# Optimization experiments

Measured on AMD Instinct MI355X. Metric: run time of the kernel, lower is better.

## Reference

```python
import jax, jax.numpy as jnp
import numpy as np

B, T, S, D, V = 32, 2048, 256, 1024, 56
STAR_PENALTY = -1.0
NEG = -1e30  # -inf surrogate that is safe for gradients


def setup_inputs() -> dict:
    key = jax.random.key(0)
    k1, k2, k3 = jax.random.split(key, 3)
    features = jax.random.normal(k1, (B, T, D), jnp.float32)
    targets = jax.random.randint(k2, (B, S), 1, V)  # 0 is the blank; labels in [1, V)
    W = jax.random.normal(k3, (V, D), jnp.float32) * (1.0 / 32.0)  # 1/sqrt(D)
    b = jnp.zeros((V,), jnp.float32)
    input_lengths = jnp.full((B,), T, jnp.int32)
    target_lengths = jnp.full((B,), S, jnp.int32)
    return dict(features=features, W=W, b=b, targets=targets,
                input_lengths=input_lengths, target_lengths=target_lengths)


def _star_ctc_losses(logp, targets, input_lengths, target_lengths, star_penalty):
    """Star-CTC forward (DP) score.
    logp: (T, N, C) log-softmax emissions; targets: (N, S) labels (blank=0 excluded).
    Extended state sequence [*, t1, *, t2, ..., tS, *]: star states play the role of
    CTC blanks but act as penalized wildcards, emitting logsumexp(logp)+star_penalty
    (== star_penalty for normalized log-probs). Standard CTC transition topology:
    self-loop, advance by 1, advance by 2 into a token state when it differs from the
    previous token. Returns per-sequence negative log-likelihood, shape (N,)."""
    Tlen, N, C = logp.shape
    Slen = targets.shape[1]
    L = 2 * Slen + 1
    ext = jnp.zeros((N, L), targets.dtype).at[:, 1::2].set(targets)  # (N, L)
    is_star = (jnp.arange(L) % 2 == 0)[None, :]                      # (1, L)
    prev2 = jnp.pad(ext[:, :-2], ((0, 0), (2, 0)), constant_values=-1)
    allow_skip = (~is_star) & (ext != prev2)                         # (N, L)

    def emit(logp_t):  # logp_t: (N, C) -> (N, L)
        star_e = star_penalty + jax.nn.logsumexp(logp_t, axis=-1, keepdims=True)
        tok_e = jnp.take_along_axis(logp_t, ext, axis=-1)
        return jnp.where(is_star, star_e, tok_e)

    alpha0 = jnp.where(jnp.arange(L)[None, :] < 2, emit(logp[0]), NEG)

    def step(alpha, xs):
        logp_t, t = xs
        a1 = jnp.pad(alpha[:, :-1], ((0, 0), (1, 0)), constant_values=NEG)
        a2 = jnp.where(allow_skip,
                       jnp.pad(alpha[:, :-2], ((0, 0), (2, 0)), constant_values=NEG),
                       NEG)
        new = jnp.logaddexp(jnp.logaddexp(alpha, a1), a2) + emit(logp_t)
        new = jnp.where(t < input_lengths[:, None], new, alpha)  # freeze past input_length
        return new, None

    alpha, _ = jax.lax.scan(step, alpha0, (logp[1:], jnp.arange(1, Tlen)))
    last = 2 * target_lengths                  # index of the final star state
    rows = jnp.arange(N)
    score = jnp.logaddexp(alpha[rows, last], alpha[rows, last - 1])
    return -score


def reference(features, W, b, targets, input_lengths, target_lengths):
    # classifier + log_softmax (Dropout(0.2) is identity at eval time)
    logits = jnp.einsum('btd,vd->btv', features, W) + b
    logp = jax.nn.log_softmax(logits.astype(jnp.float32), axis=-1)
    logp = jnp.transpose(logp, (1, 0, 2))      # (T, N, C) as in logits.permute(1,0,2)
    losses = _star_ctc_losses(logp, targets, input_lengths, target_lengths, STAR_PENALTY)
    # ctc_reduce_mean: length-normalized mean loss
    return jnp.mean(losses / target_lengths.astype(losses.dtype))
```

## Files before the change

### kernel.cpp

```cpp
#include <hip/hip_runtime.h>
#include <hip/hip_bf16.h>
#include <math.h>

typedef __attribute__((ext_vector_type(4))) float f32x4;
typedef __attribute__((ext_vector_type(8))) short s16x8;

#define LOG2E 1.4426950408889634f
#define LN2f  0.6931471805599453f
#define INV_E 0.36787944117144233f

__device__ __forceinline__ short bfc(float x) {
  unsigned u = __float_as_uint(x);
  unsigned r = u + 0x7fffu + ((u >> 16) & 1u);
  return (short)(r >> 16);
}

__device__ __forceinline__ unsigned pk2(float x, float y) {
  union { __hip_bfloat162 h; unsigned u; } c;
  c.h = __float22bfloat162_rn(make_float2(x, y));
  return c.u;
}

__device__ __forceinline__ float rdlane(float v, int lane) {
  return __int_as_float(__builtin_amdgcn_readlane(__float_as_int(v), lane));
}

__device__ __forceinline__ float pick9(int j, float a0, float a1, float a2,
                                       float a3, float a4, float a5, float a6,
                                       float a7, float a8) {
  float v = a0;
  if (j == 1) v = a1;
  if (j == 2) v = a2;
  if (j == 3) v = a3;
  if (j == 4) v = a4;
  if (j == 5) v = a5;
  if (j == 6) v = a6;
  if (j == 7) v = a7;
  if (j == 8) v = a8;
  return v;
}

__global__ void conv_w(const float* __restrict__ W, short* __restrict__ Wb,
                       int V, int D) {
  int idx = blockIdx.x * blockDim.x + threadIdx.x;
  if (idx >= 64 * D) return;
  int row = idx / D, col = idx - row * D;
  Wb[idx] = (row < V) ? bfc(W[(size_t)row * D + col]) : (short)0;
}

__global__ __launch_bounds__(256, 1) void fused_gemm_star(
    const float* __restrict__ feat, const short* __restrict__ Wb,
    const float* __restrict__ bias, float* __restrict__ ptg,
    float* __restrict__ skb, int* __restrict__ flags,
    const int* __restrict__ targets, const int* __restrict__ in_len,
    const int* __restrict__ tgt_len, float* __restrict__ partial,
    int nrows, int D, int V, int T, int S, int B, int CPB) {

  __shared__ float gbuf[4][4][64];

  if ((int)blockIdx.x >= B) {
    const int NPROD = gridDim.x - B;
    const int NTILES = B * CPB;
    const int lane = threadIdx.x & 63;
    const int wave = threadIdx.x >> 6;
    const int m_lo = lane & 15;
    const int q = lane >> 4;
    const size_t bstr = (size_t)16 * D;

    for (int i = blockIdx.x - B; i < NTILES; i += NPROD) {
      const int c = i / B;
      const int b = i - c * B;
      const int tc0 = c * 128;
      const int rlen = (T - tc0 < 128) ? (T - tc0) : 128;
      const int rowlim = b * T + tc0 + rlen;
      const int rowbase = b * T + tc0 + wave * 32;

      const int* tg = targets + (size_t)b * S;
      const int l0 = lane * 4;
      const int g1 = (l0 < S) ? tg[l0] : 0;
      const int g3 = (l0 + 1 < S) ? tg[l0 + 1] : 0;
      const int g5 = (l0 + 2 < S) ? tg[l0 + 2] : 0;
      const int g7 = (l0 + 3 < S) ? tg[l0 + 3] : 0;

      int arow0 = rowbase + m_lo;
      int arow1 = rowbase + 16 + m_lo;
      if (arow0 >= nrows) arow0 = nrows - 1;
      if (arow1 >= nrows) arow1 = nrows - 1;
      const short* Bp = Wb + (size_t)m_lo * D + q * 8;

      f32x4 acc[2][4];
      #pragma unroll
      for (int g = 0; g < 2; ++g)
        #pragma unroll
        for (int ni = 0; ni < 4; ++ni) acc[g][ni] = (f32x4){0.f, 0.f, 0.f, 0.f};

      const float* Ap0 = feat + (size_t)arow0 * D + q * 8;
      const float* Ap1 = feat + (size_t)arow1 * D + q * 8;
      float4 al0 = *(const float4*)(Ap0);
      float4 ah0 = *(const float4*)(Ap0 + 4);
      float4 al1 = *(const float4*)(Ap1);
      float4 ah1 = *(const float4*)(Ap1 + 4);
      s16x8 b0 = *(const s16x8*)(Bp);
      s16x8 b1 = *(const s16x8*)(Bp + bstr);
      s16x8 b2 = *(const s16x8*)(Bp + 2 * bstr);
      s16x8 b3 = *(const s16x8*)(Bp + 3 * bstr);

      for (int k0 = 0; k0 < D; k0 += 32) {
        const int kn = (k0 + 32 < D) ? (k0 + 32) : 0;
        const float* Ap0n = feat + (size_t)arow0 * D + kn + q * 8;
        const float* Ap1n = feat + (size_t)arow1 * D + kn + q * 8;
        const short* Bpn = Wb + (size_t)m_lo * D + kn + q * 8;
        float4 nal0 = *(const float4*)(Ap0n);
        float4 nah0 = *(const float4*)(Ap0n + 4);
        float4 nal1 = *(const float4*)(Ap1n);
        float4 nah1 = *(const float4*)(Ap1n + 4);
        s16x8 nb0 = *(const s16x8*)(Bpn);
        s16x8 nb1 = *(const s16x8*)(Bpn + bstr);
        s16x8 nb2 = *(const s16x8*)(Bpn + 2 * bstr);
        s16x8 nb3 = *(const s16x8*)(Bpn + 3 * bstr);

        union { s16x8 v; unsigned u[4]; } av0, av1;
        av0.u[0] = pk2(al0.x, al0.y); av0.u[1] = pk2(al0.z, al0.w);
        av0.u[2] = pk2(ah0.x, ah0.y); av0.u[3] = pk2(ah0.z, ah0.w);
        av1.u[0] = pk2(al1.x, al1.y); av1.u[1] = pk2(al1.z, al1.w);
        av1.u[2] = pk2(ah1.x, ah1.y); av1.u[3] = pk2(ah1.z, ah1.w);

        acc[0][0] = __builtin_amdgcn_mfma_f32_16x16x32_bf16(av0.v, b0, acc[0][0], 0, 0, 0);
        acc[0][1] = __builtin_amdgcn_mfma_f32_16x16x32_bf16(av0.v, b1, acc[0][1], 0, 0, 0);
        acc[0][2] = __builtin_amdgcn_mfma_f32_16x16x32_bf16(av0.v, b2, acc[0][2], 0, 0, 0);
        acc[0][3] = __builtin_amdgcn_mfma_f32_16x16x32_bf16(av0.v, b3, acc[0][3], 0, 0, 0);
        acc[1][0] = __builtin_amdgcn_mfma_f32_16x16x32_bf16(av1.v, b0, acc[1][0], 0, 0, 0);
        acc[1][1] = __builtin_amdgcn_mfma_f32_16x16x32_bf16(av1.v, b1, acc[1][1], 0, 0, 0);
        acc[1][2] = __builtin_amdgcn_mfma_f32_16x16x32_bf16(av1.v, b2, acc[1][2], 0, 0, 0);
        acc[1][3] = __builtin_amdgcn_mfma_f32_16x16x32_bf16(av1.v, b3, acc[1][3], 0, 0, 0);

        al0 = nal0; ah0 = nah0; al1 = nal1; ah1 = nah1;
        b0 = nb0; b1 = nb1; b2 = nb2; b3 = nb3;
      }

      float bias_v[4];
      #pragma unroll
      for (int ni = 0; ni < 4; ++ni) {
        int col = ni * 16 + m_lo;
        bias_v[ni] = (col < V) ? bias[col] : 0.f;
      }

      #pragma unroll
      for (int g = 0; g < 2; ++g) {
        #pragma unroll
        for (int r = 0; r < 4; ++r) {
          float lg[4];
          #pragma unroll
          for (int ni = 0; ni < 4; ++ni) {
            int col = ni * 16 + m_lo;
            lg[ni] = (col < V) ? (acc[g][ni][r] + bias_v[ni]) : -1e30f;
          }
          float m = fmaxf(fmaxf(lg[0], lg[1]), fmaxf(lg[2], lg[3]));
          #pragma unroll
          for (int off = 1; off < 16; off <<= 1) m = fmaxf(m, __shfl_xor(m, off));
          float p[4];
          #pragma unroll
          for (int ni = 0; ni < 4; ++ni) p[ni] = exp2f((lg[ni] - m) * LOG2E);
          float s = (p[0] + p[1]) + (p[2] + p[3]);
          #pragma unroll
          for (int off = 1; off < 16; off <<= 1) s += __shfl_xor(s, off);

          #pragma unroll
          for (int ni = 0; ni < 4; ++ni)
            gbuf[wave][q][ni * 16 + m_lo] = p[ni];

          #pragma unroll
          for (int rr = 0; rr < 4; ++rr) {
            int grow = rowbase + g * 16 + rr * 4 + r;
            if (grow < rowlim) {
              float srow = rdlane(s, rr * 16);
              float4 ev;
              ev.x = gbuf[wave][rr][g1];
              ev.y = gbuf[wave][rr][g3];
              ev.z = gbuf[wave][rr][g5];
              ev.w = gbuf[wave][rr][g7];
              *(float4*)(ptg + ((size_t)grow * 64 + lane) * 4) = ev;
              if (lane == 0) {
                float2 skv;
                skv.x = srow * INV_E;
                skv.y = logf(srow);
                *(float2*)(skb + (size_t)grow * 2) = skv;
              }
            }
          }
        }
      }

      __syncthreads();
      if (threadIdx.x == 0)
        __hip_atomic_store(&flags[b * CPB + c], 1, __ATOMIC_RELEASE,
                           __HIP_MEMORY_SCOPE_AGENT);
    }
    return;
  }

  if (threadIdx.x >= 64) return;
  const int n = blockIdx.x;
  const int lane = threadIdx.x;
  const int len = in_len[n];
  const int tl = tgt_len[n];
  const int* tg = targets + (size_t)n * S;
  const int* fl = flags + n * CPB;
  const float* prow = ptg + (size_t)n * T * 256;
  const float* srow = skb + (size_t)n * T * 2;

  int cdone = -1;
#define WAITC(cc)                                                            \
  do {                                                                       \
    int _c = (cc);                                                           \
    if (cdone < _c) {                                                        \
      while (cdone < _c) {                                                   \
        if (__hip_atomic_load((int*)&fl[cdone + 1], __ATOMIC_RELAXED,        \
                              __HIP_MEMORY_SCOPE_AGENT))                     \
          ++cdone;                                                           \
        else                                                                 \
          __builtin_amdgcn_s_sleep(8);                                       \
      }                                                                      \
      __builtin_amdgcn_fence(__ATOMIC_ACQUIRE, "agent");                     \
    }                                                                        \
  } while (0)

  const int s0 = lane * 4;
  int lab1 = (s0     < S) ? tg[s0]     : 0;
  int lab3 = (s0 + 1 < S) ? tg[s0 + 1] : 0;
  int lab5 = (s0 + 2 < S) ? tg[s0 + 2] : 0;
  int lab7 = (s0 + 3 < S) ? tg[s0 + 3] : 0;
  int labm1 = __shfl_up(lab7, 1);
  int labm3 = __shfl_up(lab5, 1);
  const bool sk1 = (lane > 0) && (lab1 != labm1);
  const bool sk3 = (lab3 != lab1);
  const bool sk5 = (lab5 != lab3);
  const bool sk7 = (lab7 != lab5);
  const bool skm1 = (labm1 != labm3);

  float a0 = 0, a1 = 0, a2 = 0, a3 = 0, a4 = 0, a5 = 0, a6 = 0, a7 = 0, a8 = 0;
  float m1 = 0.f, m2 = 0.f, m3 = 0.f;
  int eps = 0, eL = 0;
  bool act = (lane == 0);

#define PTGL(t) (*(const float4*)(prow +                                     \
    ((size_t)(((t) < len) ? (t) : (len - 1)) * 256 + lane * 4)))
#define SKLL(t) (*(const float2*)(srow +                                     \
    ((size_t)(((t) < len) ? (t) : (len - 1)) * 2)))

  WAITC(0);

  float4 r0 = PTGL(0);
  float2 k0v = SKLL(0);
  if (lane == 0) { a0 = k0v.x; a1 = r0.x; }
  float ksum = k0v.y;

  float4 rr0 = PTGL(1), rr1 = PTGL(2), rr2 = PTGL(3), rr3 = PTGL(4);
  float4 rr4 = PTGL(5), rr5 = PTGL(6), rr6 = PTGL(7), rr7 = PTGL(8);
  float2 kr0 = SKLL(1), kr1 = SKLL(2), kr2 = SKLL(3), kr3 = SKLL(4);
  float2 kr4 = SKLL(5), kr5 = SKLL(6), kr6 = SKLL(7), kr7 = SKLL(8);

  float em1a = __shfl_up(rr0.w, 1);

#define RENORM()                                                             \
  do {                                                                       \
    float mx = fmaxf(fmaxf(fmaxf(a0, a1), fmaxf(a2, a3)),                    \
                     fmaxf(fmaxf(a4, a5), fmaxf(a6, a7)));                   \
    mx = fmaxf(mx, a8);                                                      \
    int e = (int)((__float_as_uint(mx) >> 23) & 255) - 126;                  \
    e = (act && mx > 0.f) ? e : 0;                                           \
    a0 = ldexpf(a0, -e); a1 = ldexpf(a1, -e); a2 = ldexpf(a2, -e);           \
    a3 = ldexpf(a3, -e); a4 = ldexpf(a4, -e); a5 = ldexpf(a5, -e);           \
    a6 = ldexpf(a6, -e); a7 = ldexpf(a7, -e); a8 = ldexpf(a8, -e);           \
    eps += e;                                                                \
  } while (0)

#define PAIR(EC0, EC1, KC0, KC1, NX, P0, P1, DOREN)                          \
  do {                                                                       \
    ksum += KC0.y; ksum += KC1.y;                                            \
    if (!act) eps = eL;                                                      \
    bool inc = (lane != 0) &&                                                \
               ((m1 != 0.f) || (m2 != 0.f) || (m3 != 0.f));                  \
    int d = inc ? (eL - eps) : 0;                                            \
    if (__builtin_expect(d > 24, 0)) {                  \
      a0 = ldexpf(a0, -d); a1 = ldexpf(a1, -d); a2 = ldexpf(a2, -d);         \
      a3 = ldexpf(a3, -d); a4 = ldexpf(a4, -d); a5 = ldexpf(a5, -d);         \
      a6 = ldexpf(a6, -d); a7 = ldexpf(a7, -d); a8 = ldexpf(a8, -d);         \
      eps += d;                                      \
    } else {                                                                 \
      m1 = ldexpf(m1, d); m2 = ldexpf(m2, d); m3 = ldexpf(m3, d);            \
    }                                                                        \
    act = act || (m1 != 0.f) || (m2 != 0.f) || (m3 != 0.f);                  \
                  \
    a8 = (a8 + a7) * KC0.x;                                                  \
    a7 = (a7 + a6 + (sk7 ? a5 : 0.f)) * EC0.w;                               \
    a6 = (a6 + a5) * KC0.x;                                                  \
    a5 = (a5 + a4 + (sk5 ? a3 : 0.f)) * EC0.z;                               \
    a4 = (a4 + a3) * KC0.x;                                                  \
    a3 = (a3 + a2 + (sk3 ? a1 : 0.f)) * EC0.y;                               \
    a2 = (a2 + a1) * KC0.x;                                                  \
    a1 = (a1 + a0 + (sk1 ? m1 : 0.f)) * EC0.x;                               \
    a0 = (a0 + m1) * KC0.x;                                                  \
    m1 = (m1 + m2 + (skm1 ? m3 : 0.f)) * em1a;                               \
                                                             \
    a8 = (a8 + a7) * KC1.x;                                                  \
    a7 = (a7 + a6 + (sk7 ? a5 : 0.f)) * EC1.w;                               \
    a6 = (a6 + a5) * KC1.x;                                                  \
    a5 = (a5 + a4 + (sk5 ? a3 : 0.f)) * EC1.z;                               \
    a4 = (a4 + a3) * KC1.x;                                                  \
    a3 = (a3 + a2 + (sk3 ? a1 : 0.f)) * EC1.y;                               \
    a2 = (a2 + a1) * KC1.x;                                                  \
    a1 = (a1 + a0 + (sk1 ? m1 : 0.f)) * EC1.x;                               \
    a0 = (a0 + m1) * KC1.x;                                                  \
    EC0 = PTGL(P0); EC1 = PTGL(P1);                   \
    KC0 = SKLL(P0); KC1 = SKLL(P1);                                          \
    if (DOREN) RENORM();                                                     \
    em1a = __shfl_up(NX.w, 1);                     \
                          \
    m3 = __shfl_up(a5, 1); m2 = __shfl_up(a6, 1); m1 = __shfl_up(a7, 1);     \
    eL = __shfl_up(eps, 1);                                                  \
    if (lane == 0) { m1 = 0.f; m2 = 0.f; m3 = 0.f; }                         \
  } while (0)

  int t0 = 1;
  for (; t0 + 8 <= len; t0 += 8) {
    int tmax = t0 + 15;
    if (tmax > len - 1) tmax = len - 1;
    WAITC(tmax >> 7);
    PAIR(rr0, rr1, kr0, kr1, rr2, t0 + 8,  t0 + 9,  false);
    PAIR(rr2, rr3, kr2, kr3, rr4, t0 + 10, t0 + 11, false);
    PAIR(rr4, rr5, kr4, kr5, rr6, t0 + 12, t0 + 13, false);
    PAIR(rr6, rr7, kr6, kr7, rr0, t0 + 14, t0 + 15, true);
  }

  WAITC((len - 1) >> 7);

  for (int t = t0; t < len; ++t) {
    float4 cv = PTGL(t);
    float2 kc = SKLL(t);
    ksum += kc.y;
    if (!act) eps = eL;
    bool inc = (lane != 0) && (m1 != 0.f);
    int d = inc ? (eL - eps) : 0;
    float m1s;
    if (__builtin_expect(d > 24, 0)) {
      a0 = ldexpf(a0, -d); a1 = ldexpf(a1, -d); a2 = ldexpf(a2, -d);
      a3 = ldexpf(a3, -d); a4 = ldexpf(a4, -d); a5 = ldexpf(a5, -d);
      a6 = ldexpf(a6, -d); a7 = ldexpf(a7, -d); a8 = ldexpf(a8, -d);
      eps += d; m1s = m1;
    } else {
      m1s = inc ? ldexpf(m1, d) : 0.f;
    }
    act = act || (m1s != 0.f);
    a8 = (a8 + a7) * kc.x;
    a7 = (a7 + a6 + (sk7 ? a5 : 0.f)) * cv.w;
    a6 = (a6 + a5) * kc.x;
    a5 = (a5 + a4 + (sk5 ? a3 : 0.f)) * cv.z;
    a4 = (a4 + a3) * kc.x;
    a3 = (a3 + a2 + (sk3 ? a1 : 0.f)) * cv.y;
    a2 = (a2 + a1) * kc.x;
    a1 = (a1 + a0 + (sk1 ? m1s : 0.f)) * cv.x;
    a0 = (a0 + m1s) * kc.x;
    if ((t & 7) == 0) RENORM();
    m1 = __shfl_up(a7, 1);
    eL = __shfl_up(eps, 1);
    if (lane == 0) m1 = 0.f;
  }

  int last = 2 * tl;
  int kx = last >> 3, jx = last & 7;
  if (kx > 63) { kx = 63; jx = last - 504; }
  int ky = (last - 1) >> 3, jy = (last - 1) & 7;
  float vx = pick9(jx, a0, a1, a2, a3, a4, a5, a6, a7, a8);
  float vy = pick9(jy, a0, a1, a2, a3, a4, a5, a6, a7, a8);
  float sx = __shfl(vx, kx); int ex = __shfl(eps, kx);
  float sy = __shfl(vy, ky); int ey = __shfl(eps, ky);
  if (lane == 0) {
    int em = (ex > ey) ? ex : ey;
    float v = ldexpf(sx, ex - em) + ldexpf(sy, ey - em);
    float score = logf(v) + (float)em * LN2f - ksum;
    partial[n] = -score / (float)tl;
  }
#undef WAITC
#undef PTGL
#undef SKLL
#undef RENORM
#undef PAIR
}

__global__ void reduce_mean(const float* __restrict__ partial,
                            float* __restrict__ out, int B) {
  float v = 0.f;
  for (int i = threadIdx.x; i < B; i += 64) v += partial[i];
  #pragma unroll
  for (int off = 32; off > 0; off >>= 1) v += __shfl_down(v, off, 64);
  if (threadIdx.x == 0) out[0] = v / (float)B;
}

extern "C" void kernel_launch(void* const* d_in, const int* in_sizes, int n_in,
                              void* d_out, int out_size, void* d_ws, size_t ws_size,
                              hipStream_t stream) {
  const float* feat = (const float*)d_in[0];
  const float* W = (const float*)d_in[1];
  const float* bias = (const float*)d_in[2];
  const int* targets = (const int*)d_in[3];
  const int* in_len = (const int*)d_in[4];
  const int* tgt_len = (const int*)d_in[5];
  float* out = (float*)d_out;

  const int V = in_sizes[2];
  const int D = in_sizes[1] / V;
  const int B = in_sizes[4];
  const int T = in_sizes[0] / (B * D);
  const int S = in_sizes[3] / B;
  const int nrows = B * T;

  float* ptg = (float*)d_ws;
  float* skb = ptg + (size_t)nrows * 256;
  float* partial = skb + (size_t)nrows * 2;
  short* Wb = (short*)(partial + B);
  const int CPB = (T + 127) / 128;
  int* flags = (int*)((char*)Wb + (size_t)64 * D * sizeof(short));

  hipMemsetAsync(flags, 0, (size_t)B * CPB * sizeof(int), stream);

  conv_w<<<(64 * D + 255) / 256, 256, 0, stream>>>(W, Wb, V, D);

  int NPROD = 256 - B;
  const int NTILES = B * CPB;
  if (NPROD > NTILES) NPROD = NTILES;
  fused_gemm_star<<<dim3(B + NPROD), 256, 0, stream>>>(
      feat, Wb, bias, ptg, skb, flags, targets, in_len, tgt_len, partial,
      nrows, D, V, T, S, B, CPB);

  reduce_mean<<<1, 64, 0, stream>>>(partial, out, B);
}
```

Measured before the change: 715.1 us.

## Launch one producer block per tile with deeper load prefetch and fused flag reset

Producer blocks no longer loop over tiles persistently: the grid now has one block per (batch, chunk) tile, and launch bounds allow two blocks per CU. The GEMM K-loop keeps a four-stage register prefetch instead of one stage, so more global loads are in flight to hide memory latency. The flag memset is folded into the weight-conversion kernel to drop a separate launch. The risk is scheduling: consumer blocks spin-wait on flags, so if producer blocks are dispatched ahead of consumers or starve them, forward progress depends on dispatch order. Register pressure also rises from the extra prefetch buffers while the occupancy target is higher.

```diff
diff --git a/kernel.cpp b/kernel.cpp
--- a/kernel.cpp
+++ b/kernel.cpp
@@ -41,14 +41,15 @@
 }
 
 __global__ void conv_w(const float* __restrict__ W, short* __restrict__ Wb,
-                       int V, int D) {
+                       int V, int D, int* __restrict__ flags, int nflags) {
   int idx = blockIdx.x * blockDim.x + threadIdx.x;
+  if (idx < nflags) flags[idx] = 0;
   if (idx >= 64 * D) return;
   int row = idx / D, col = idx - row * D;
   Wb[idx] = (row < V) ? bfc(W[(size_t)row * D + col]) : (short)0;
 }
 
-__global__ __launch_bounds__(256, 1) void fused_gemm_star(
+__global__ __launch_bounds__(256, 2) void fused_gemm_star(
     const float* __restrict__ feat, const short* __restrict__ Wb,
     const float* __restrict__ bias, float* __restrict__ ptg,
     float* __restrict__ skb, int* __restrict__ flags,
@@ -59,143 +60,149 @@
   __shared__ float gbuf[4][4][64];
 
   if ((int)blockIdx.x >= B) {
-    const int NPROD = gridDim.x - B;
-    const int NTILES = B * CPB;
+    const int j = blockIdx.x - B;
+    const int c = j / B;
+    const int b = j - c * B;
+    const int tc0 = c * 128;
+    const int rlen = (T - tc0 < 128) ? (T - tc0) : 128;
+    const int rowlim = b * T + tc0 + rlen;
+
     const int lane = threadIdx.x & 63;
     const int wave = threadIdx.x >> 6;
     const int m_lo = lane & 15;
     const int q = lane >> 4;
     const size_t bstr = (size_t)16 * D;
-
-    for (int i = blockIdx.x - B; i < NTILES; i += NPROD) {
-      const int c = i / B;
-      const int b = i - c * B;
-      const int tc0 = c * 128;
-      const int rlen = (T - tc0 < 128) ? (T - tc0) : 128;
-      const int rowlim = b * T + tc0 + rlen;
-      const int rowbase = b * T + tc0 + wave * 32;
-
-      const int* tg = targets + (size_t)b * S;
-      const int l0 = lane * 4;
-      const int g1 = (l0 < S) ? tg[l0] : 0;
-      const int g3 = (l0 + 1 < S) ? tg[l0 + 1] : 0;
-      const int g5 = (l0 + 2 < S) ? tg[l0 + 2] : 0;
-      const int g7 = (l0 + 3 < S) ? tg[l0 + 3] : 0;
-
-      int arow0 = rowbase + m_lo;
-      int arow1 = rowbase + 16 + m_lo;
-      if (arow0 >= nrows) arow0 = nrows - 1;
-      if (arow1 >= nrows) arow1 = nrows - 1;
-      const short* Bp = Wb + (size_t)m_lo * D + q * 8;
-
-      f32x4 acc[2][4];
+    const int rowbase = b * T + tc0 + wave * 32;
+
+    const int* tg = targets + (size_t)b * S;
+    const int l0 = lane * 4;
+    const int g1 = (l0 < S) ? tg[l0] : 0;
+    const int g3 = (l0 + 1 < S) ? tg[l0 + 1] : 0;
+    const int g5 = (l0 + 2 < S) ? tg[l0 + 2] : 0;
+    const int g7 = (l0 + 3 < S) ? tg[l0 + 3] : 0;
+
+    int arow0 = rowbase + m_lo;
+    int arow1 = rowbase + 16 + m_lo;
+    if (arow0 >= nrows) arow0 = nrows - 1;
+    if (arow1 >= nrows) arow1 = nrows - 1;
+    const float* A0base = feat + (size_t)arow0 * D + q * 8;
+    const float* A1base = feat + (size_t)arow1 * D + q * 8;
+    const short* Bbase = Wb + (size_t)m_lo * D + q * 8;
+
+    f32x4 acc[2][4];
+    #pragma unroll
+    for (int g = 0; g < 2; ++g)
       #pragma unroll
-      for (int g = 0; g < 2; ++g)
-        #pragma unroll
-        for (int ni = 0; ni < 4; ++ni) acc[g][ni] = (f32x4){0.f, 0.f, 0.f, 0.f};
-
-      const float* Ap0 = feat + (size_t)arow0 * D + q * 8;
-      const float* Ap1 = feat + (size_t)arow1 * D + q * 8;
-      float4 al0 = *(const float4*)(Ap0);
-      float4 ah0 = *(const float4*)(Ap0 + 4);
-      float4 al1 = *(const float4*)(Ap1);
-      float4 ah1 = *(const float4*)(Ap1 + 4);
-      s16x8 b0 = *(const s16x8*)(Bp);
-      s16x8 b1 = *(const s16x8*)(Bp + bstr);
-      s16x8 b2 = *(const s16x8*)(Bp + 2 * bstr);
-      s16x8 b3 = *(const s16x8*)(Bp + 3 * bstr);
-
-      for (int k0 = 0; k0 < D; k0 += 32) {
-        const int kn = (k0 + 32 < D) ? (k0 + 32) : 0;
-        const float* Ap0n = feat + (size_t)arow0 * D + kn + q * 8;
-        const float* Ap1n = feat + (size_t)arow1 * D + kn + q * 8;
-        const short* Bpn = Wb + (size_t)m_lo * D + kn + q * 8;
-        float4 nal0 = *(const float4*)(Ap0n);
-        float4 nah0 = *(const float4*)(Ap0n + 4);
-        float4 nal1 = *(const float4*)(Ap1n);
-        float4 nah1 = *(const float4*)(Ap1n + 4);
-        s16x8 nb0 = *(const s16x8*)(Bpn);
-        s16x8 nb1 = *(const s16x8*)(Bpn + bstr);
-        s16x8 nb2 = *(const s16x8*)(Bpn + 2 * bstr);
-        s16x8 nb3 = *(const s16x8*)(Bpn + 3 * bstr);
-
-        union { s16x8 v; unsigned u[4]; } av0, av1;
-        av0.u[0] = pk2(al0.x, al0.y); av0.u[1] = pk2(al0.z, al0.w);
-        av0.u[2] = pk2(ah0.x, ah0.y); av0.u[3] = pk2(ah0.z, ah0.w);
-        av1.u[0] = pk2(al1.x, al1.y); av1.u[1] = pk2(al1.z, al1.w);
-        av1.u[2] = pk2(ah1.x, ah1.y); av1.u[3] = pk2(ah1.z, ah1.w);
-
-        acc[0][0] = __builtin_amdgcn_mfma_f32_16x16x32_bf16(av0.v, b0, acc[0][0], 0, 0, 0);
-        acc[0][1] = __builtin_amdgcn_mfma_f32_16x16x32_bf16(av0.v, b1, acc[0][1], 0, 0, 0);
-        acc[0][2] = __builtin_amdgcn_mfma_f32_16x16x32_bf16(av0.v, b2, acc[0][2], 0, 0, 0);
-        acc[0][3] = __builtin_amdgcn_mfma_f32_16x16x32_bf16(av0.v, b3, acc[0][3], 0, 0, 0);
-        acc[1][0] = __builtin_amdgcn_mfma_f32_16x16x32_bf16(av1.v, b0, acc[1][0], 0, 0, 0);
-        acc[1][1] = __builtin_amdgcn_mfma_f32_16x16x32_bf16(av1.v, b1, acc[1][1], 0, 0, 0);
-        acc[1][2] = __builtin_amdgcn_mfma_f32_16x16x32_bf16(av1.v, b2, acc[1][2], 0, 0, 0);
-        acc[1][3] = __builtin_amdgcn_mfma_f32_16x16x32_bf16(av1.v, b3, acc[1][3], 0, 0, 0);
-
-        al0 = nal0; ah0 = nah0; al1 = nal1; ah1 = nah1;
-        b0 = nb0; b1 = nb1; b2 = nb2; b3 = nb3;
-      }
-
-      float bias_v[4];
+      for (int ni = 0; ni < 4; ++ni) acc[g][ni] = (f32x4){0.f, 0.f, 0.f, 0.f};
+
+#define DECLS(s) float4 al0_##s, ah0_##s, al1_##s, ah1_##s;                  \
+                 s16x8 b0_##s, b1_##s, b2_##s, b3_##s
+    DECLS(0); DECLS(1); DECLS(2); DECLS(3);
+#undef DECLS
+
+#define LOADS(s, kk)                                                         \
+  do {                                                                       \
+    const float* A0p = A0base + (kk);                                        \
+    const float* A1p = A1base + (kk);                                        \
+    const short* Bpp = Bbase + (kk);                                         \
+    al0_##s = *(const float4*)(A0p);                                         \
+    ah0_##s = *(const float4*)(A0p + 4);                                     \
+    al1_##s = *(const float4*)(A1p);                                         \
+    ah1_##s = *(const float4*)(A1p + 4);                                     \
+    b0_##s = *(const s16x8*)(Bpp);                                           \
+    b1_##s = *(const s16x8*)(Bpp + bstr);                                    \
+    b2_##s = *(const s16x8*)(Bpp + 2 * bstr);                                \
+    b3_##s = *(const s16x8*)(Bpp + 3 * bstr);                                \
+  } while (0)
+
+#define COMPUTE(s)                                                           \
+  do {                                                                       \
+    union { s16x8 v; unsigned u[4]; } av0, av1;                              \
+    av0.u[0] = pk2(al0_##s.x, al0_##s.y);                                    \
+    av0.u[1] = pk2(al0_##s.z, al0_##s.w);                                    \
+    av0.u[2] = pk2(ah0_##s.x, ah0_##s.y);                                    \
+    av0.u[3] = pk2(ah0_##s.z, ah0_##s.w);                                    \
+    av1.u[0] = pk2(al1_##s.x, al1_##s.y);                                    \
+    av1.u[1] = pk2(al1_##s.z, al1_##s.w);                                    \
+    av1.u[2] = pk2(ah1_##s.x, ah1_##s.y);                                    \
+    av1.u[3] = pk2(ah1_##s.z, ah1_##s.w);                                    \
+    acc[0][0] = __builtin_amdgcn_mfma_f32_16x16x32_bf16(av0.v, b0_##s, acc[0][0], 0, 0, 0); \
+    acc[0][1] = __builtin_amdgcn_mfma_f32_16x16x32_bf16(av0.v, b1_##s, acc[0][1], 0, 0, 0); \
+    acc[0][2] = __builtin_amdgcn_mfma_f32_16x16x32_bf16(av0.v, b2_##s, acc[0][2], 0, 0, 0); \
+    acc[0][3] = __builtin_amdgcn_mfma_f32_16x16x32_bf16(av0.v, b3_##s, acc[0][3], 0, 0, 0); \
+    acc[1][0] = __builtin_amdgcn_mfma_f32_16x16x32_bf16(av1.v, b0_##s, acc[1][0], 0, 0, 0); \
+    acc[1][1] = __builtin_amdgcn_mfma_f32_16x16x32_bf16(av1.v, b1_##s, acc[1][1], 0, 0, 0); \
+    acc[1][2] = __builtin_amdgcn_mfma_f32_16x16x32_bf16(av1.v, b2_##s, acc[1][2], 0, 0, 0); \
+    acc[1][3] = __builtin_amdgcn_mfma_f32_16x16x32_bf16(av1.v, b3_##s, acc[1][3], 0, 0, 0); \
+  } while (0)
+
+    LOADS(0, 0); LOADS(1, 32); LOADS(2, 64); LOADS(3, 96);
+    for (int k0 = 0; k0 < D; k0 += 128) {
+      { COMPUTE(0); int kp = k0 + 128; if (kp >= D) kp = 0;  LOADS(0, kp); }
+      { COMPUTE(1); int kp = k0 + 160; if (kp >= D) kp = 32; LOADS(1, kp); }
+      { COMPUTE(2); int kp = k0 + 192; if (kp >= D) kp = 64; LOADS(2, kp); }
+      { COMPUTE(3); int kp = k0 + 224; if (kp >= D) kp = 96; LOADS(3, kp); }
+    }
+#undef LOADS
+#undef COMPUTE
+
+    float bias_v[4];
+    #pragma unroll
+    for (int ni = 0; ni < 4; ++ni) {
+      int col = ni * 16 + m_lo;
+      bias_v[ni] = (col < V) ? bias[col] : 0.f;
+    }
+
+    #pragma unroll
+    for (int g = 0; g < 2; ++g) {
       #pragma unroll
-      for (int ni = 0; ni < 4; ++ni) {
-        int col = ni * 16 + m_lo;
-        bias_v[ni] = (col < V) ? bias[col] : 0.f;
-      }
-
-      #pragma unroll
-      for (int g = 0; g < 2; ++g) {
-        #pragma unroll
-        for (int r = 0; r < 4; ++r) {
-          float lg[4];
-          #pragma unroll
-          for (int ni = 0; ni < 4; ++ni) {
-            int col = ni * 16 + m_lo;
-            lg[ni] = (col < V) ? (acc[g][ni][r] + bias_v[ni]) : -1e30f;
-          }
-          float m = fmaxf(fmaxf(lg[0], lg[1]), fmaxf(lg[2], lg[3]));
-          #pragma unroll
-          for (int off = 1; off < 16; off <<= 1) m = fmaxf(m, __shfl_xor(m, off));
-          float p[4];
-          #pragma unroll
-          for (int ni = 0; ni < 4; ++ni) p[ni] = exp2f((lg[ni] - m) * LOG2E);
-          float s = (p[0] + p[1]) + (p[2] + p[3]);
-          #pragma unroll
-          for (int off = 1; off < 16; off <<= 1) s += __shfl_xor(s, off);
-
-          #pragma unroll
-          for (int ni = 0; ni < 4; ++ni)
-            gbuf[wave][q][ni * 16 + m_lo] = p[ni];
-
-          #pragma unroll
-          for (int rr = 0; rr < 4; ++rr) {
-            int grow = rowbase + g * 16 + rr * 4 + r;
-            if (grow < rowlim) {
-              float srow = rdlane(s, rr * 16);
-              float4 ev;
-              ev.x = gbuf[wave][rr][g1];
-              ev.y = gbuf[wave][rr][g3];
-              ev.z = gbuf[wave][rr][g5];
-              ev.w = gbuf[wave][rr][g7];
-              *(float4*)(ptg + ((size_t)grow * 64 + lane) * 4) = ev;
-              if (lane == 0) {
-                float2 skv;
-                skv.x = srow * INV_E;
-                skv.y = logf(srow);
-                *(float2*)(skb + (size_t)grow * 2) = skv;
-              }
+      for (int r = 0; r < 4; ++r) {
+        float lg[4];
+        #pragma unroll
+        for (int ni = 0; ni < 4; ++ni) {
+          int col = ni * 16 + m_lo;
+          lg[ni] = (col < V) ? (acc[g][ni][r] + bias_v[ni]) : -1e30f;
+        }
+        float m = fmaxf(fmaxf(lg[0], lg[1]), fmaxf(lg[2], lg[3]));
+        #pragma unroll
+        for (int off = 1; off < 16; off <<= 1) m = fmaxf(m, __shfl_xor(m, off));
+        float p[4];
+        #pragma unroll
+        for (int ni = 0; ni < 4; ++ni) p[ni] = exp2f((lg[ni] - m) * LOG2E);
+        float s = (p[0] + p[1]) + (p[2] + p[3]);
+        #pragma unroll
+        for (int off = 1; off < 16; off <<= 1) s += __shfl_xor(s, off);
+
+        #pragma unroll
+        for (int ni = 0; ni < 4; ++ni)
+          gbuf[wave][q][ni * 16 + m_lo] = p[ni];
+
+        #pragma unroll
+        for (int rr = 0; rr < 4; ++rr) {
+          int grow = rowbase + g * 16 + rr * 4 + r;
+          if (grow < rowlim) {
+            float srow = rdlane(s, rr * 16);
+            float4 ev;
+            ev.x = gbuf[wave][rr][g1];
+            ev.y = gbuf[wave][rr][g3];
+            ev.z = gbuf[wave][rr][g5];
+            ev.w = gbuf[wave][rr][g7];
+            *(float4*)(ptg + ((size_t)grow * 64 + lane) * 4) = ev;
+            if (lane == 0) {
+              float2 skv;
+              skv.x = srow * INV_E;
+              skv.y = logf(srow);
+              *(float2*)(skb + (size_t)grow * 2) = skv;
             }
           }
         }
       }
-
-      __syncthreads();
-      if (threadIdx.x == 0)
-        __hip_atomic_store(&flags[b * CPB + c], 1, __ATOMIC_RELEASE,
-                           __HIP_MEMORY_SCOPE_AGENT);
     }
+
+    __syncthreads();
+    if (threadIdx.x == 0)
+      __hip_atomic_store(&flags[b * CPB + c], 1, __ATOMIC_RELEASE,
+                         __HIP_MEMORY_SCOPE_AGENT);
     return;
   }
 
@@ -422,14 +429,11 @@
   const int CPB = (T + 127) / 128;
   int* flags = (int*)((char*)Wb + (size_t)64 * D * sizeof(short));
 
-  hipMemsetAsync(flags, 0, (size_t)B * CPB * sizeof(int), stream);
-
-  conv_w<<<(64 * D + 255) / 256, 256, 0, stream>>>(W, Wb, V, D);
-
-  int NPROD = 256 - B;
+  conv_w<<<(64 * D + 255) / 256, 256, 0, stream>>>(W, Wb, V, D,
+                                                   flags, B * CPB);
+
   const int NTILES = B * CPB;
-  if (NPROD > NTILES) NPROD = NTILES;
-  fused_gemm_star<<<dim3(B + NPROD), 256, 0, stream>>>(
+  fused_gemm_star<<<dim3(B + NTILES), 256, 0, stream>>>(
       feat, Wb, bias, ptg, skb, flags, targets, in_len, tgt_len, partial,
       nrows, D, V, T, S, B, CPB);
 
```

Result: slower. 760.3 us (+6.3%).
